# Performance work log

Measured on AMD Instinct MI355X. Metric: run time of the kernel, lower is better.

Reference implementation:

```python
import jax, jax.numpy as jnp
import numpy as np

N_WAY = 5
K_SHOT = 5
TEMPERATURE = 2.0
EPS = 1e-8


def _l2norm(x, axis):
    n = jnp.sqrt(jnp.sum(x * x, axis=axis, keepdims=True))
    return x / jnp.maximum(n, EPS)


def setup_inputs() -> dict:
    key = jax.random.key(0)
    k1, k2, k3, k4 = jax.random.split(key, 4)
    b, q, c, h, w = 4, 75, 640, 14, 14
    s = N_WAY * K_SHOT
    return {
        "support_xf": jax.random.normal(k1, (b, s, c, h, w), dtype=jnp.float32),
        "support_y": jax.random.randint(k2, (b, s), 0, N_WAY),
        "query_xf": jax.random.normal(k3, (b, q, c, h, w), dtype=jnp.float32),
        "query_y": jax.random.randint(k4, (b, q), 0, N_WAY),
    }


def _mn4_loss(support_xf, query_xf, query_y):
    b, q, c, h, w = query_xf.shape
    M = h * w  # M_q == M_s (k_shot averaging)
    # k-shot average: (b, N, k, c, h*w) -> (b, N, c, M)
    sup = support_xf.reshape(b, N_WAY, K_SHOT, c, M).mean(axis=2)
    qf = query_xf.reshape(b, q, c, M)
    # cosine similarity: normalize along channel dim
    sup_n = _l2norm(sup, axis=2)   # (b, N, c, M)
    qf_n = _l2norm(qf, axis=2)     # (b, q, c, M)
    # S: (b, q, N, M_q, M_s)
    S = jnp.einsum('bqcm,bncs->bqnms', qf_n, sup_n)

    NM = N_WAY * M
    # merged: (b, q, M_q, N*M_s)
    merged = jnp.transpose(S, (0, 1, 3, 2, 4)).reshape(b, q, M, NM)
    query_nearest = jnp.argmax(merged, axis=-1)               # (b, q, M_q)
    class_wise_max = S.max(axis=-1).max(axis=2) + 1.0          # (b, q, M_q)
    class_m = jax.nn.one_hot(query_nearest, NM, dtype=S.dtype) * class_wise_max[..., None]  # (b,q,M_q,NM)
    class_m_max = class_m.max(axis=-2)                         # (b, q, NM)
    support_nearest = jnp.argmax(class_m, axis=-2)             # (b, q, NM)
    support_nearest = jnp.where(class_m_max == 0, M + 1, support_nearest)
    # gather: back-pointer for each query position's chosen support index
    gathered = jnp.take_along_axis(support_nearest, query_nearest, axis=-1)  # (b, q, M_q)
    mask = (gathered == jnp.arange(M)[None, None, :])          # mutual-NN mask (b, q, M_q)
    query_mask = mask.astype(S.dtype) * TEMPERATURE

    # predict: masked sum of per-class best similarities over query positions
    predict = (S.max(axis=-1) * query_mask[:, :, None, :]).sum(axis=-1)  # (b, q, N)
    predict = predict.reshape(b * q, N_WAY)
    y = query_y.reshape(b * q)
    logp = jax.nn.log_softmax(predict, axis=-1)
    loss = -jnp.take_along_axis(logp, y[:, None], axis=1).mean()
    return loss


def reference(support_xf, support_y, query_xf, query_y):
    return _mn4_loss(support_xf, query_xf, query_y)
```

## Files before the change

kernel.cpp:

```cpp
#include <hip/hip_runtime.h>
#include <math.h>

#define NWAY 5
#define KSHOT 5
#define BB 4
#define QQ 75
#define CC 640
#define MM 196
#define BQ (BB*QQ)
#define MP 208
#define NCOL 1024
#define NREAL 980

#define BPK_OFF   0
#define BPK_SZF   (BB*NCOL*CC/2)
#define APK_OFF   (BPK_OFF + BPK_SZF)
#define APK_SZF   ((BQ*MP + 64)*CC/2)
#define GSTAT_OFF (APK_OFF + APK_SZF)
#define GSTAT_N   (BQ*NWAY*MP)
#define NRMS_OFF  (GSTAT_OFF + 2*GSTAT_N)
#define NRMS_SZ   (BB*NWAY*MM)
#define NRMQ_OFF  (NRMS_OFF + NRMS_SZ)
#define NRMQ_SZ   (BQ*MM)

typedef __attribute__((ext_vector_type(8))) _Float16 half8;
typedef __attribute__((ext_vector_type(4))) float floatx4;

__global__ void k_prep(const float* __restrict__ sx, const float* __restrict__ qx,
                       _Float16* __restrict__ Apk, _Float16* __restrict__ Bpk,
                       float* __restrict__ nrmq, float* __restrict__ nrms) {
    __shared__ float T[64 * 197];
    int t = threadIdx.x;
    int blk = blockIdx.x;
    if (blk < 3000) {
        int bq = blk / 10, cc = blk % 10;
        int c0 = cc * 64;
        const float* Q = qx + (size_t)bq * CC * MM + (size_t)c0 * MM;
        for (int idx = t; idx < 64 * MM; idx += 256) {
            int ci = idx / MM, m = idx - ci * MM;
            T[ci * 197 + m] = Q[idx];
        }
        __syncthreads();
        _Float16* out = Apk + (size_t)bq * MP * CC;
        int mloc = t >> 3, cj8 = t & 7;
        #pragma unroll
        for (int r = 0; r < 7; r++) {
            int mm = r * 32 + mloc;
            if (mm < MP) {
                half8 v;
                #pragma unroll
                for (int k = 0; k < 8; k++) {
                    float f = (mm < MM) ? T[(cj8 * 8 + k) * 197 + mm] : 0.f;
                    v[k] = (_Float16)f;
                }
                *(half8*)&out[(size_t)mm * CC + c0 + cj8 * 8] = v;
            }
        }
        if (t < MM) {
            float ss = 0.f;
            for (int ci = 0; ci < 64; ci++) { float v = T[ci * 197 + t]; ss += v * v; }
            atomicAdd(&nrmq[bq * MM + t], ss);
        }
    } else {
        int bb = blk - 3000;
        int bn = bb / 10, cc = bb % 10;
        int b = bn / NWAY, n = bn % NWAY;
        int c0 = cc * 64;
        const float* S = sx + (size_t)bn * KSHOT * CC * MM + (size_t)c0 * MM;
        for (int idx = t; idx < 64 * MM; idx += 256) {
            int ci = idx / MM, m = idx - ci * MM;
            float s = 0.f;
            #pragma unroll
            for (int k = 0; k < KSHOT; k++) s += S[(size_t)k * CC * MM + idx];
            T[ci * 197 + m] = s * 0.2f;
        }
        __syncthreads();
        _Float16* out = Bpk + ((size_t)b * NCOL + (size_t)n * MM) * CC;
        int mloc = t >> 3, cj8 = t & 7;
        #pragma unroll
        for (int r = 0; r < 7; r++) {
            int mm = r * 32 + mloc;
            if (mm < MM) {
                half8 v;
                #pragma unroll
                for (int k = 0; k < 8; k++)
                    v[k] = (_Float16)T[(cj8 * 8 + k) * 197 + mm];
                *(half8*)&out[(size_t)mm * CC + c0 + cj8 * 8] = v;
            }
        }
        if (t < MM) {
            float ss = 0.f;
            for (int ci = 0; ci < 64; ci++) { float v = T[ci * 197 + t]; ss += v * v; }
            atomicAdd(&nrms[bn * MM + t], ss);
        }
    }
}

__global__ __launch_bounds__(512, 2) void k_sim(
    const _Float16* __restrict__ Apk, const _Float16* __restrict__ Bpk,
    const float* __restrict__ nrms, unsigned long long* __restrict__ gstat)
{
    __shared__ __align__(16) _Float16 Lds[65536];

    int hw = blockIdx.x;
    int logical = (hw & 7) * 150 + (hw >> 3);
    int bq = logical >> 2, cblk = logical & 3;
    int b = bq / QQ;

    int t = threadIdx.x, w = t >> 6, lane = t & 63;
    int wm = w >> 2, wn = w & 3;
    int q = lane >> 4, l15 = lane & 15, s7 = l15 & 7;

    const _Float16* Ab = Apk + (size_t)bq * MP * CC;
    const _Float16* Bb = Bpk + ((size_t)b * NCOL + (size_t)cblk * 256) * CC;

    int voff[4];
    {
        int rr = t >> 3, slot = t & 7;
        #pragma unroll
        for (int a = 0; a < 4; a++) {
            int r = a * 64 + rr;
            voff[a] = r * CC + ((slot ^ (r & 7)) << 3);
        }
    }

    int aoff[8], boff[4];
    #pragma unroll
    for (int m = 0; m < 8; m++) aoff[m] = (wm * 128 + m * 16 + l15) * 64;
    #pragma unroll
    for (int n = 0; n < 4; n++) boff[n] = 16384 + (wn * 64 + n * 16 + l15) * 64;

    floatx4 acc[8][4];
    #pragma unroll
    for (int m = 0; m < 8; m++)
        #pragma unroll
        for (int n = 0; n < 4; n++) acc[m][n] = (floatx4){0.f, 0.f, 0.f, 0.f};

    #define STAGE(TT)                                                                  \
        do {                                                                           \
            int nb_ = ((TT) & 1) << 15;                                                \
            int c0_ = (TT) * 64;                                                       \
            _Pragma("unroll")                                                          \
            for (int a = 0; a < 4; a++) {                                              \
                __builtin_amdgcn_global_load_lds(                                      \
                    (const __attribute__((address_space(1))) void*)(Ab + voff[a] + c0_),\
                    (__attribute__((address_space(3))) void*)(Lds + nb_ + a * 4096 + w * 512), \
                    16, 0, 0);                                                         \
                __builtin_amdgcn_global_load_lds(                                      \
                    (const __attribute__((address_space(1))) void*)(Bb + voff[a] + c0_),\
                    (__attribute__((address_space(3))) void*)(Lds + nb_ + 16384 + a * 4096 + w * 512), \
                    16, 0, 0);                                                         \
            }                                                                          \
        } while (0)

    STAGE(0);
    __syncthreads();

    for (int tt = 0; tt < 10; tt++) {
        int cb = (tt & 1) << 15;
        if (tt < 9) STAGE(tt + 1);

        half8 bf[4][2];
        #pragma unroll
        for (int n = 0; n < 4; n++)
            #pragma unroll
            for (int ks = 0; ks < 2; ks++)
                bf[n][ks] = *(const half8*)&Lds[cb + boff[n] + (((ks * 4 + q) ^ s7) << 3)];

        __builtin_amdgcn_s_setprio(1);
        #define MFMA_BLOCK(MTOP)                                                       \
            _Pragma("unroll")                                                          \
            for (int m = 0; m < (MTOP); m++) {                                         \
                half8 af0 = *(const half8*)&Lds[cb + aoff[m] + ((q ^ s7) << 3)];       \
                half8 af1 = *(const half8*)&Lds[cb + aoff[m] + (((4 + q) ^ s7) << 3)]; \
                _Pragma("unroll")                                                      \
                for (int n = 0; n < 4; n++) {                                          \
                    acc[m][n] = __builtin_amdgcn_mfma_f32_16x16x32_f16(af0, bf[n][0], acc[m][n], 0, 0, 0); \
                    acc[m][n] = __builtin_amdgcn_mfma_f32_16x16x32_f16(af1, bf[n][1], acc[m][n], 0, 0, 0); \
                }                                                                      \
            }
        if (wm == 0) { MFMA_BLOCK(8) } else { MFMA_BLOCK(5) }
        __builtin_amdgcn_s_setprio(0);

        __syncthreads();
    }

    int wbase = cblk * 256 + wn * 64;
    int clsLo = wbase / 196;
    int clsHi = clsLo + 1;
    bool hasHi = (((wbase + 63) / 196) != clsLo) && (clsHi < NWAY);
    float invv[4]; int msv[4], isLo[4], valid[4];
    #pragma unroll
    for (int n = 0; n < 4; n++) {
        int c = wbase + n * 16 + l15;
        int cls = c / 196;
        msv[n] = c - cls * 196;
        isLo[n] = (cls == clsLo);
        valid[n] = (c < NREAL);
        invv[n] = valid[n] ? (1.0f / fmaxf(sqrtf(nrms[b * NREAL + c]), 1e-8f)) : 0.f;
    }
    #pragma unroll
    for (int m = 0; m < 8; m++) {
        if (wm == 1 && m >= 5) continue;
        #pragma unroll
        for (int r = 0; r < 4; r++) {
            unsigned long long keyLo = 0ULL, keyHi = 0ULL;
            #pragma unroll
            for (int n = 0; n < 4; n++) {
                float v = acc[m][n][r] * invv[n];
                unsigned int ub = __float_as_uint(v);
                unsigned int su = (ub & 0x80000000u) ? ~ub : (ub | 0x80000000u);
                unsigned long long key = valid[n]
                    ? (((unsigned long long)su << 32) |
                       (unsigned long long)(0xFFFFFFFFu - (unsigned int)msv[n]))
                    : 0ULL;
                if (isLo[n]) keyLo = (key > keyLo) ? key : keyLo;
                else         keyHi = (key > keyHi) ? key : keyHi;
            }
            #pragma unroll
            for (int sft = 1; sft < 16; sft <<= 1) {
                unsigned long long o = __shfl_xor(keyLo, sft, 64);
                if (o > keyLo) keyLo = o;
            }
            if (hasHi) {
                #pragma unroll
                for (int sft = 1; sft < 16; sft <<= 1) {
                    unsigned long long o = __shfl_xor(keyHi, sft, 64);
                    if (o > keyHi) keyHi = o;
                }
            }
            if (l15 == 0) {
                int gm = wm * 128 + m * 16 + q * 4 + r;
                if (gm < MM) {
                    if (keyLo)
                        atomicMax(&gstat[((size_t)bq * NWAY + clsLo) * MP + gm], keyLo);
                    if (hasHi && keyHi)
                        atomicMax(&gstat[((size_t)bq * NWAY + clsHi) * MP + gm], keyHi);
                }
            }
        }
    }
}

__global__ void k_post(const unsigned long long* __restrict__ gstat,
                       const float* __restrict__ nrmq,
                       float* __restrict__ out, const int* __restrict__ qy) {
    int bq = blockIdx.x;
    int t = threadIdx.x;
    __shared__ float invq_s[MM];
    __shared__ float cm[NWAY * MM];
    __shared__ int   ca[NWAY * MM];
    __shared__ float gmax[MM];
    __shared__ int   jst[MM];
    __shared__ int   msk[MM];
    __shared__ float pred[NWAY];

    if (t < MM) invq_s[t] = 1.0f / fmaxf(sqrtf(nrmq[bq * MM + t]), 1e-8f);
    __syncthreads();

    for (int i = t; i < NWAY * MM; i += 256) {
        int n = i / MM, m = i - n * MM;
        unsigned long long key = gstat[((size_t)bq * NWAY + n) * MP + m];
        unsigned int hi = (unsigned int)(key >> 32);
        unsigned int bits = (hi & 0x80000000u) ? (hi ^ 0x80000000u) : ~hi;
        cm[i] = __uint_as_float(bits) * invq_s[m];
        ca[i] = (int)(0xFFFFFFFFu - (unsigned int)(key & 0xFFFFFFFFu));
    }
    __syncthreads();

    if (t < MM) {
        float bv = cm[t];
        int bj = ca[t];
        for (int n = 1; n < NWAY; n++) {
            float v = cm[n * MM + t];
            if (v > bv) { bv = v; bj = n * MM + ca[n * MM + t]; }
        }
        gmax[t] = bv; jst[t] = bj;
    }
    __syncthreads();

    if (t < MM) {
        int myj = jst[t];
        float myv = gmax[t];
        int lose = 0;
        for (int m2 = 0; m2 < MM; m2++) {
            if (jst[m2] == myj &&
                (gmax[m2] > myv || (gmax[m2] == myv && m2 < t))) lose = 1;
        }
        msk[t] = !lose;
    }
    __syncthreads();

    if (t < NWAY) {
        float p = 0.f;
        for (int m = 0; m < MM; m++) if (msk[m]) p += cm[t * MM + m];
        pred[t] = 2.0f * p;
    }
    __syncthreads();

    if (t == 0) {
        float pm = pred[0];
        for (int n = 1; n < NWAY; n++) pm = fmaxf(pm, pred[n]);
        float s = 0.f;
        for (int n = 0; n < NWAY; n++) s += expf(pred[n] - pm);
        float lse = pm + logf(s);
        int y = qy[bq];
        atomicAdd(out, (lse - pred[y]) * (1.0f / (BB * QQ)));
    }
}

extern "C" void kernel_launch(void* const* d_in, const int* in_sizes, int n_in,
                              void* d_out, int out_size, void* d_ws, size_t ws_size,
                              hipStream_t stream) {
    const float* sx = (const float*)d_in[0];
    const float* qx = (const float*)d_in[2];
    const int*   qy = (const int*)d_in[3];
    float* out = (float*)d_out;
    float* ws  = (float*)d_ws;

    _Float16* Bpk = (_Float16*)(ws + BPK_OFF);
    _Float16* Apk = (_Float16*)(ws + APK_OFF);
    unsigned long long* gstat = (unsigned long long*)(ws + GSTAT_OFF);
    float* nrms = ws + NRMS_OFF;
    float* nrmq = ws + NRMQ_OFF;

    hipMemsetAsync(gstat, 0, (size_t)(2 * GSTAT_N + NRMS_SZ + NRMQ_SZ) * 4, stream);
    hipMemsetAsync(out, 0, 4, stream);
    hipLaunchKernelGGL(k_prep, dim3(3200), dim3(256), 0, stream, sx, qx, Apk, Bpk, nrmq, nrms);
    hipLaunchKernelGGL(k_sim,  dim3(1200), dim3(512), 0, stream, Apk, Bpk, nrms, gstat);
    hipLaunchKernelGGL(k_post, dim3(300), dim3(256), 0, stream, gstat, nrmq, out, qy);
}
```

Before: 465.6 us.

## Split GEMM K-step into four quadrant phases with explicit barriers and waits

Restructures the inner GEMM loop so each K-tile is processed in four quadrant phases (A half × B half). Each phase reads its A and B fragments from LDS, then waits on lgkmcnt and runs MFMAs, with raw s_barrier calls separating phases. The aim is to shrink register pressure, since fragments now take 4x2 plus 2x2 instead of 4x2 per B and streamed A. It also aims to interleave LDS reads with MFMA across waves in a ping-pong style. The cost is many more barriers per iteration, plus a re-read of the A fragments in the last phase, which adds LDS traffic.

Measured after the change: 483.2 us. 3.8% more time.

```diff
diff --git a/kernel.cpp b/kernel.cpp
--- a/kernel.cpp
+++ b/kernel.cpp
@@ -136,6 +136,8 @@
         #pragma unroll
         for (int n = 0; n < 4; n++) acc[m][n] = (floatx4){0.f, 0.f, 0.f, 0.f};
 
+    half8 af[4][2], bf[2][2];
+
     #define STAGE(TT)                                                                  \
         do {                                                                           \
             int nb_ = ((TT) & 1) << 15;                                                \
@@ -153,36 +155,85 @@
             }                                                                          \
         } while (0)
 
+    #define BARR() __builtin_amdgcn_s_barrier()
+    #define WAIT_LGKM0() do { asm volatile("s_waitcnt lgkmcnt(0)" ::: "memory"); \
+                              __builtin_amdgcn_sched_barrier(0); } while (0)
+    #define WAIT_VM0()   do { asm volatile("s_waitcnt vmcnt(0)" ::: "memory");   \
+                              __builtin_amdgcn_sched_barrier(0); } while (0)
+
+    #define READ_AF(MH)                                                                \
+        _Pragma("unroll")                                                              \
+        for (int mi = 0; mi < 4; mi++)                                                 \
+            _Pragma("unroll")                                                          \
+            for (int ks = 0; ks < 2; ks++)                                             \
+                af[mi][ks] = *(const half8*)&Lds[cb + aoff[(MH)*4+mi] + (((ks*4+q)^s7)<<3)];
+    #define READ_AF1_TRIM()                                                            \
+        _Pragma("unroll")                                                              \
+        for (int ks = 0; ks < 2; ks++)                                                 \
+            af[0][ks] = *(const half8*)&Lds[cb + aoff[4] + (((ks*4+q)^s7)<<3)];
+    #define READ_BF(NH)                                                                \
+        _Pragma("unroll")                                                              \
+        for (int ni = 0; ni < 2; ni++)                                                 \
+            _Pragma("unroll")                                                          \
+            for (int ks = 0; ks < 2; ks++)                                             \
+                bf[ni][ks] = *(const half8*)&Lds[cb + boff[(NH)*2+ni] + (((ks*4+q)^s7)<<3)];
+    #define MFMA_Q(MH,NH)                                                              \
+        _Pragma("unroll")                                                              \
+        for (int mi = 0; mi < 4; mi++)                                                 \
+            _Pragma("unroll")                                                          \
+            for (int ni = 0; ni < 2; ni++)                                             \
+                _Pragma("unroll")                                                      \
+                for (int ks = 0; ks < 2; ks++)                                         \
+                    acc[(MH)*4+mi][(NH)*2+ni] = __builtin_amdgcn_mfma_f32_16x16x32_f16( \
+                        af[mi][ks], bf[ni][ks], acc[(MH)*4+mi][(NH)*2+ni], 0, 0, 0);
+    #define MFMA_Q1_TRIM(NH)                                                           \
+        _Pragma("unroll")                                                              \
+        for (int ni = 0; ni < 2; ni++)                                                 \
+            _Pragma("unroll")                                                          \
+            for (int ks = 0; ks < 2; ks++)                                             \
+                acc[4][(NH)*2+ni] = __builtin_amdgcn_mfma_f32_16x16x32_f16(            \
+                    af[0][ks], bf[ni][ks], acc[4][(NH)*2+ni], 0, 0, 0);
+
     STAGE(0);
-    __syncthreads();
+    WAIT_VM0();
+    BARR();
 
     for (int tt = 0; tt < 10; tt++) {
         int cb = (tt & 1) << 15;
+
+        READ_AF(0); READ_BF(0);
         if (tt < 9) STAGE(tt + 1);
-
-        half8 bf[4][2];
-        #pragma unroll
-        for (int n = 0; n < 4; n++)
-            #pragma unroll
-            for (int ks = 0; ks < 2; ks++)
-                bf[n][ks] = *(const half8*)&Lds[cb + boff[n] + (((ks * 4 + q) ^ s7) << 3)];
-
+        BARR();
+        WAIT_LGKM0();
         __builtin_amdgcn_s_setprio(1);
-        #define MFMA_BLOCK(MTOP)                                                       \
-            _Pragma("unroll")                                                          \
-            for (int m = 0; m < (MTOP); m++) {                                         \
-                half8 af0 = *(const half8*)&Lds[cb + aoff[m] + ((q ^ s7) << 3)];       \
-                half8 af1 = *(const half8*)&Lds[cb + aoff[m] + (((4 + q) ^ s7) << 3)]; \
-                _Pragma("unroll")                                                      \
-                for (int n = 0; n < 4; n++) {                                          \
-                    acc[m][n] = __builtin_amdgcn_mfma_f32_16x16x32_f16(af0, bf[n][0], acc[m][n], 0, 0, 0); \
-                    acc[m][n] = __builtin_amdgcn_mfma_f32_16x16x32_f16(af1, bf[n][1], acc[m][n], 0, 0, 0); \
-                }                                                                      \
-            }
-        if (wm == 0) { MFMA_BLOCK(8) } else { MFMA_BLOCK(5) }
+        MFMA_Q(0, 0);
         __builtin_amdgcn_s_setprio(0);
-
-        __syncthreads();
+        BARR();
+
+        if (wm == 0) { READ_AF(1); } else { READ_AF1_TRIM(); }
+        BARR();
+        WAIT_LGKM0();
+        __builtin_amdgcn_s_setprio(1);
+        if (wm == 0) { MFMA_Q(1, 0); } else { MFMA_Q1_TRIM(0); }
+        __builtin_amdgcn_s_setprio(0);
+        BARR();
+
+        READ_BF(1);
+        BARR();
+        WAIT_LGKM0();
+        __builtin_amdgcn_s_setprio(1);
+        if (wm == 0) { MFMA_Q(1, 1); } else { MFMA_Q1_TRIM(1); }
+        __builtin_amdgcn_s_setprio(0);
+        BARR();
+
+        READ_AF(0);
+        BARR();
+        WAIT_LGKM0();
+        __builtin_amdgcn_s_setprio(1);
+        MFMA_Q(0, 1);
+        __builtin_amdgcn_s_setprio(0);
+        WAIT_VM0();
+        BARR();
     }
 
     int wbase = cblk * 256 + wn * 64;
```
